# Kernel tuning notes

Hardware: AMD Instinct MI355X
Metric: run time of the kernel (lower is better)

Reference implementation:

```python
import jax, jax.numpy as jnp
import numpy as np

N, E, D, L = 100000, 640000, 128, 5
BN_EPS = 1e-5


def setup_inputs() -> dict:
    key = jax.random.key(0)
    ks = jax.random.split(key, 10)
    x = jax.random.normal(ks[0], (N, D), jnp.float32)
    edge_index = jax.random.randint(ks[1], (2, E), 0, N, dtype=jnp.int32)
    W1 = jax.random.normal(ks[2], (L, D, 2 * D), jnp.float32) / np.float32(np.sqrt(D))
    b1 = jnp.zeros((L, 2 * D), jnp.float32)
    bn1_g = jnp.ones((L, 2 * D), jnp.float32)
    bn1_b = jnp.zeros((L, 2 * D), jnp.float32)
    bn1_m = 0.1 * jax.random.normal(ks[3], (L, 2 * D), jnp.float32)
    bn1_v = jax.random.uniform(ks[4], (L, 2 * D), jnp.float32) + 0.5
    W2 = jax.random.normal(ks[5], (L, 2 * D, D), jnp.float32) / np.float32(np.sqrt(2 * D))
    b2 = jnp.zeros((L, D), jnp.float32)
    bno_g = jnp.ones((L, D), jnp.float32)
    bno_b = jnp.zeros((L, D), jnp.float32)
    bno_m = 0.1 * jax.random.normal(ks[6], (L, D), jnp.float32)
    bno_v = jax.random.uniform(ks[7], (L, D), jnp.float32) + 0.5
    return {"x": x, "edge_index": edge_index, "W1": W1, "b1": b1,
            "bn1_g": bn1_g, "bn1_b": bn1_b, "bn1_m": bn1_m, "bn1_v": bn1_v,
            "W2": W2, "b2": b2,
            "bno_g": bno_g, "bno_b": bno_b, "bno_m": bno_m, "bno_v": bno_v}


def _bn(z, g, b, m, v):
    # BatchNorm1d in eval mode: running stats
    return (z - m) * jax.lax.rsqrt(v + BN_EPS) * g + b


def reference(x, edge_index, W1, b1, bn1_g, bn1_b, bn1_m, bn1_v,
              W2, b2, bno_g, bno_b, bno_m, bno_v):
    src, dst = edge_index[0], edge_index[1]
    h = x
    for l in range(L):
        # GINConv with eps=0: (1+eps)*h_i + sum_{j->i} h_j
        agg = h + jax.ops.segment_sum(h[src], dst, num_segments=N)  # [N, d]
        z = jax.nn.relu(_bn(agg @ W1[l] + b1[l], bn1_g[l], bn1_b[l], bn1_m[l], bn1_v[l]))
        h = _bn(z @ W2[l] + b2[l], bno_g[l], bno_b[l], bno_m[l], bno_v[l])
        if l != L - 1:
            h = jax.nn.relu(h)
        # dropout is identity in eval mode
    return h
```

## Files before the change

kernel.cpp:

```cpp
#include <hip/hip_runtime.h>

#define ND 100000
#define DD 128
#define HH 256
#define EE 640000
#define LL 5

#define GS 152
#define ZS 280
#define OS 136
#define OF 132

typedef __attribute__((ext_vector_type(8))) short short8;
typedef __attribute__((ext_vector_type(4))) short short4v;
typedef __attribute__((ext_vector_type(4))) float f32x4;

static __device__ __forceinline__ short f2bf(float f) {
    unsigned u = __builtin_bit_cast(unsigned, f);
    unsigned r = (u + 0x7fffu + ((u >> 16) & 1u)) >> 16;
    return (short)r;
}
static __device__ __forceinline__ float bf2f(short s) {
    unsigned u = ((unsigned)(unsigned short)s) << 16;
    return __builtin_bit_cast(float, u);
}

__global__ __launch_bounds__(256) void setup(
    const float* __restrict__ W1, const float* __restrict__ b1,
    const float* __restrict__ g1, const float* __restrict__ bb1,
    const float* __restrict__ m1, const float* __restrict__ v1,
    const float* __restrict__ W2, const float* __restrict__ b2,
    const float* __restrict__ g2, const float* __restrict__ bb2,
    const float* __restrict__ m2, const float* __restrict__ v2,
    const float* __restrict__ x, const int* __restrict__ dst,
    short* __restrict__ W1p, float* __restrict__ b1e,
    short* __restrict__ W2p, float* __restrict__ b2e,
    short* __restrict__ hb, int* __restrict__ cnt)
{
    int bx = blockIdx.x;
    int tid = threadIdx.x;
    if (bx < 640) {
        int id = bx * 256 + tid;
        if (id < LL * HH * DD) {
            int l = id >> 15;
            int rem = id & 32767;
            {
                int n = rem >> 7, k = rem & 127;
                float s = g1[l * HH + n] * rsqrtf(v1[l * HH + n] + 1e-5f);
                W1p[id] = f2bf(W1[l * 32768 + k * HH + n] * s);
            }
            {
                int n2 = rem >> 8, k2 = rem & 255;
                float s = g2[l * DD + n2] * rsqrtf(v2[l * DD + n2] + 1e-5f);
                W2p[id] = f2bf(W2[l * 32768 + k2 * DD + n2] * s);
            }
        }
        if (id < LL * HH) {
            float s = g1[id] * rsqrtf(v1[id] + 1e-5f);
            b1e[id] = (b1[id] - m1[id]) * s + bb1[id];
        }
        if (id < LL * DD) {
            float s = g2[id] * rsqrtf(v2[id] + 1e-5f);
            b2e[id] = (b2[id] - m2[id]) * s + bb2[id];
        }
    } else if (bx < 13140) {
        int i = (bx - 640) * 256 + tid;
        float4 v = reinterpret_cast<const float4*>(x)[i];
        short4v s;
        s.x = f2bf(v.x); s.y = f2bf(v.y); s.z = f2bf(v.z); s.w = f2bf(v.w);
        reinterpret_cast<short4v*>(hb)[i] = s;
    } else {
        int e = (bx - 13140) * 256 + tid;
        if (e < EE) atomicAdd(&cnt[dst[e]], 1);
    }
}

__global__ __launch_bounds__(256) void scan_block(int* __restrict__ cnt, int* __restrict__ bsum)
{
    __shared__ int buf[256];
    int tid = threadIdx.x;
    int idx = blockIdx.x * 256 + tid;
    int v = (idx < ND) ? cnt[idx] : 0;
    buf[tid] = v;
    __syncthreads();
    int sum = v;
    for (int off = 1; off < 256; off <<= 1) {
        int t = (tid >= off) ? buf[tid - off] : 0;
        __syncthreads();
        sum += t;
        buf[tid] = sum;
        __syncthreads();
    }
    if (idx < ND) cnt[idx] = sum;
    if (tid == 255) bsum[blockIdx.x] = sum;
}

__global__ __launch_bounds__(256) void apply_offs2(const int* __restrict__ cnt,
                                                   const int* __restrict__ bsum,
                                                   int* __restrict__ rowst)
{
    __shared__ int sred[256];
    int tid = threadIdx.x;
    int partial = 0;
    for (int i = tid; i < blockIdx.x; i += 256) partial += bsum[i];
    sred[tid] = partial;
    __syncthreads();
    for (int off = 128; off > 0; off >>= 1) {
        if (tid < off) sred[tid] += sred[tid + off];
        __syncthreads();
    }
    int boff = sred[0];
    int idx = blockIdx.x * 256 + tid;
    if (idx < ND) rowst[idx + 1] = cnt[idx] + boff;
    if (idx == 0) rowst[0] = 0;
}

__global__ __launch_bounds__(256) void fill_csr(const int* __restrict__ src,
                                                const int* __restrict__ dst,
                                                const int* __restrict__ rowstart,
                                                int* __restrict__ cursor,
                                                int* __restrict__ csr)
{
    int e = blockIdx.x * 256 + threadIdx.x;
    if (e < EE) {
        int d = dst[e];
        int p = atomicAdd(&cursor[d], 1);
        csr[rowstart[d] + p] = src[e];
    }
}

__global__ __launch_bounds__(512, 8) void layer_fused(
    const short* __restrict__ hb_in,
    const int* __restrict__ rowst,
    const int* __restrict__ csr,
    const short* __restrict__ W1l,
    const float* __restrict__ b1l,
    const short* __restrict__ W2l,
    const float* __restrict__ b2l,
    short* __restrict__ hb_out, float* __restrict__ f_out, int last)
{
    __shared__ __attribute__((aligned(16))) short sU[32 * ZS];

    const int tid = threadIdx.x;
    const int r0 = blockIdx.x * 32;
    const int w = tid >> 6;
    const int lane = tid & 63;
    const int quad = lane >> 4;
    const int l16 = lane & 15;

    {
        const int row = tid >> 4;
        const int ch = (tid & 15) * 8;
        const int grow = r0 + row;
        const int s = rowst[grow], e = rowst[grow + 1];
        short8 h0 = *reinterpret_cast<const short8*>(&hb_in[(size_t)grow * DD + ch]);
        float acc[8];
        #pragma unroll
        for (int j = 0; j < 8; ++j) acc[j] = bf2f(h0[j]);

        const int deg = e - s;
        const int nfull = deg >> 2;
        const int rem = deg & 3;
        int i = s;
        short8 ca[4];
        if (nfull) {
            #pragma unroll
            for (int k = 0; k < 4; ++k)
                ca[k] = *reinterpret_cast<const short8*>(&hb_in[(size_t)csr[i + k] * DD + ch]);
            i += 4;
            for (int b = 1; b < nfull; ++b) {
                short8 na[4];
                #pragma unroll
                for (int k = 0; k < 4; ++k)
                    na[k] = *reinterpret_cast<const short8*>(&hb_in[(size_t)csr[i + k] * DD + ch]);
                i += 4;
                #pragma unroll
                for (int j = 0; j < 8; ++j)
                    acc[j] += (bf2f(ca[0][j]) + bf2f(ca[1][j])) + (bf2f(ca[2][j]) + bf2f(ca[3][j]));
                #pragma unroll
                for (int k = 0; k < 4; ++k) ca[k] = na[k];
            }
        }
        short8 t0, t1, t2;
        if (rem > 0) t0 = *reinterpret_cast<const short8*>(&hb_in[(size_t)csr[i] * DD + ch]);
        if (rem > 1) t1 = *reinterpret_cast<const short8*>(&hb_in[(size_t)csr[i + 1] * DD + ch]);
        if (rem > 2) t2 = *reinterpret_cast<const short8*>(&hb_in[(size_t)csr[i + 2] * DD + ch]);
        if (nfull) {
            #pragma unroll
            for (int j = 0; j < 8; ++j)
                acc[j] += (bf2f(ca[0][j]) + bf2f(ca[1][j])) + (bf2f(ca[2][j]) + bf2f(ca[3][j]));
        }
        if (rem > 0) {
            #pragma unroll
            for (int j = 0; j < 8; ++j) acc[j] += bf2f(t0[j]);
        }
        if (rem > 1) {
            #pragma unroll
            for (int j = 0; j < 8; ++j) acc[j] += bf2f(t1[j]);
        }
        if (rem > 2) {
            #pragma unroll
            for (int j = 0; j < 8; ++j) acc[j] += bf2f(t2[j]);
        }
        short8 o;
        #pragma unroll
        for (int j = 0; j < 8; ++j) o[j] = f2bf(acc[j]);
        *reinterpret_cast<short8*>(&sU[row * GS + ch]) = o;
    }
    __syncthreads();

    const f32x4 zero4 = {0.f, 0.f, 0.f, 0.f};
    f32x4 acc1[2][2];
    #pragma unroll
    for (int h = 0; h < 2; ++h)
        #pragma unroll
        for (int nt = 0; nt < 2; ++nt) acc1[h][nt] = zero4;

    const int zr0 = w * 32 + l16;
    short8 a_cur0 = *reinterpret_cast<const short8*>(&W1l[zr0 * DD + quad * 8]);
    short8 a_cur1 = *reinterpret_cast<const short8*>(&W1l[(zr0 + 16) * DD + quad * 8]);

    __builtin_amdgcn_s_setprio(1);
    #pragma unroll
    for (int ks = 0; ks < 4; ++ks) {
        short8 a_n0, a_n1;
        if (ks < 3) {
            a_n0 = *reinterpret_cast<const short8*>(&W1l[zr0 * DD + (ks + 1) * 32 + quad * 8]);
            a_n1 = *reinterpret_cast<const short8*>(&W1l[(zr0 + 16) * DD + (ks + 1) * 32 + quad * 8]);
        }
        int kofs = ks * 32 + quad * 8;
        short8 b0 = *reinterpret_cast<const short8*>(&sU[l16 * GS + kofs]);
        short8 b1 = *reinterpret_cast<const short8*>(&sU[(16 + l16) * GS + kofs]);
        acc1[0][0] = __builtin_amdgcn_mfma_f32_16x16x32_bf16(a_cur0, b0, acc1[0][0], 0, 0, 0);
        acc1[0][1] = __builtin_amdgcn_mfma_f32_16x16x32_bf16(a_cur0, b1, acc1[0][1], 0, 0, 0);
        acc1[1][0] = __builtin_amdgcn_mfma_f32_16x16x32_bf16(a_cur1, b0, acc1[1][0], 0, 0, 0);
        acc1[1][1] = __builtin_amdgcn_mfma_f32_16x16x32_bf16(a_cur1, b1, acc1[1][1], 0, 0, 0);
        a_cur0 = a_n0; a_cur1 = a_n1;
    }
    __builtin_amdgcn_s_setprio(0);

    float4 bi0 = *reinterpret_cast<const float4*>(&b1l[w * 32 + quad * 4]);
    float4 bi1 = *reinterpret_cast<const float4*>(&b1l[w * 32 + 16 + quad * 4]);
    __syncthreads();

    #pragma unroll
    for (int h = 0; h < 2; ++h) {
        float4 bi = h ? bi1 : bi0;
        int zc = w * 32 + h * 16 + quad * 4;
        #pragma unroll
        for (int nt = 0; nt < 2; ++nt) {
            int node = nt * 16 + l16;
            short4v o;
            o.x = f2bf(fmaxf(acc1[h][nt][0] + bi.x, 0.f));
            o.y = f2bf(fmaxf(acc1[h][nt][1] + bi.y, 0.f));
            o.z = f2bf(fmaxf(acc1[h][nt][2] + bi.z, 0.f));
            o.w = f2bf(fmaxf(acc1[h][nt][3] + bi.w, 0.f));
            *reinterpret_cast<short4v*>(&sU[node * ZS + zc]) = o;
        }
    }

    const int orow = w * 16 + l16;
    short8 w_cur = *reinterpret_cast<const short8*>(&W2l[orow * HH + quad * 8]);
    float4 bi2 = *reinterpret_cast<const float4*>(&b2l[w * 16 + quad * 4]);
    __syncthreads();

    f32x4 acc2[2];
    acc2[0] = zero4; acc2[1] = zero4;

    __builtin_amdgcn_s_setprio(1);
    #pragma unroll
    for (int ks = 0; ks < 8; ++ks) {
        short8 w_next;
        if (ks < 7)
            w_next = *reinterpret_cast<const short8*>(&W2l[orow * HH + (ks + 1) * 32 + quad * 8]);
        int kofs = ks * 32 + quad * 8;
        short8 b0 = *reinterpret_cast<const short8*>(&sU[l16 * ZS + kofs]);
        short8 b1 = *reinterpret_cast<const short8*>(&sU[(16 + l16) * ZS + kofs]);
        acc2[0] = __builtin_amdgcn_mfma_f32_16x16x32_bf16(w_cur, b0, acc2[0], 0, 0, 0);
        acc2[1] = __builtin_amdgcn_mfma_f32_16x16x32_bf16(w_cur, b1, acc2[1], 0, 0, 0);
        w_cur = w_next;
    }
    __builtin_amdgcn_s_setprio(0);
    __syncthreads();

    const int oc = w * 16 + quad * 4;
    if (!last) {
        #pragma unroll
        for (int nt = 0; nt < 2; ++nt) {
            int node = nt * 16 + l16;
            short4v o;
            o.x = f2bf(fmaxf(acc2[nt][0] + bi2.x, 0.f));
            o.y = f2bf(fmaxf(acc2[nt][1] + bi2.y, 0.f));
            o.z = f2bf(fmaxf(acc2[nt][2] + bi2.z, 0.f));
            o.w = f2bf(fmaxf(acc2[nt][3] + bi2.w, 0.f));
            *reinterpret_cast<short4v*>(&sU[node * OS + oc]) = o;
        }
        __syncthreads();
        int row = tid >> 4;
        int c8 = (tid & 15) * 8;
        short8 v = *reinterpret_cast<const short8*>(&sU[row * OS + c8]);
        *reinterpret_cast<short8*>(&hb_out[(size_t)(r0 + row) * DD + c8]) = v;
    } else {
        float* fU = reinterpret_cast<float*>(sU);
        #pragma unroll
        for (int nt = 0; nt < 2; ++nt) {
            int node = nt * 16 + l16;
            float4 o;
            o.x = acc2[nt][0] + bi2.x;
            o.y = acc2[nt][1] + bi2.y;
            o.z = acc2[nt][2] + bi2.z;
            o.w = acc2[nt][3] + bi2.w;
            *reinterpret_cast<float4*>(&fU[node * OF + oc]) = o;
        }
        __syncthreads();
        int row = tid >> 4;
        int cb = (tid & 15) * 8;
        float4 v0 = *reinterpret_cast<const float4*>(&fU[row * OF + cb]);
        float4 v1 = *reinterpret_cast<const float4*>(&fU[row * OF + cb + 4]);
        *reinterpret_cast<float4*>(&f_out[(size_t)(r0 + row) * DD + cb]) = v0;
        *reinterpret_cast<float4*>(&f_out[(size_t)(r0 + row) * DD + cb + 4]) = v1;
    }
}

extern "C" void kernel_launch(void* const* d_in, const int* in_sizes, int n_in,
                              void* d_out, int out_size, void* d_ws, size_t ws_size,
                              hipStream_t stream)
{
    const float* x  = (const float*)d_in[0];
    const int* ei   = (const int*)d_in[1];
    const int* src  = ei;
    const int* dst  = ei + EE;
    const float* W1 = (const float*)d_in[2];
    const float* b1 = (const float*)d_in[3];
    const float* g1 = (const float*)d_in[4];
    const float* bb1= (const float*)d_in[5];
    const float* m1 = (const float*)d_in[6];
    const float* v1 = (const float*)d_in[7];
    const float* W2 = (const float*)d_in[8];
    const float* b2 = (const float*)d_in[9];
    const float* g2 = (const float*)d_in[10];
    const float* bb2= (const float*)d_in[11];
    const float* m2 = (const float*)d_in[12];
    const float* v2 = (const float*)d_in[13];

    char* w = (char*)d_ws;
    short* hbufA = (short*)w;
    short* hbufB = (short*)(w + 25600000);
    short* W1p   = (short*)(w + 51200000);
    short* W2p   = (short*)(w + 51527680);
    float* b1e   = (float*)(w + 51855360);
    float* b2e   = (float*)(w + 51860480);
    int*   cnt   = (int*)  (w + 51863040);
    int*   cursor= (int*)  (w + 52263040);
    int*   rowst = (int*)  (w + 52663040);
    int*   csr   = (int*)  (w + 53063072);
    int*   bsum  = (int*)  (w + 55623072);
    float* out   = (float*)d_out;

    hipMemsetAsync(cnt, 0, 800000, stream);
    setup<<<15640, 256, 0, stream>>>(W1, b1, g1, bb1, m1, v1,
                                     W2, b2, g2, bb2, m2, v2,
                                     x, dst, W1p, b1e, W2p, b2e, hbufA, cnt);
    scan_block<<<391, 256, 0, stream>>>(cnt, bsum);
    apply_offs2<<<391, 256, 0, stream>>>(cnt, bsum, rowst);
    fill_csr<<<2500, 256, 0, stream>>>(src, dst, rowst, cursor, csr);

    short* hin = hbufA;
    short* hout = hbufB;
    for (int l = 0; l < LL; ++l) {
        layer_fused<<<3125, 512, 0, stream>>>(hin, rowst, csr,
                                              W1p + l * 32768, b1e + l * HH,
                                              W2p + l * 32768, b2e + l * DD,
                                              hout, out, (l == LL - 1) ? 1 : 0);
        short* t = hin; hin = hout; hout = t;
    }
}
```

Baseline: 549.4 us.

## Sort nodes into degree bins so each layer block gathers rows of similar degree

```diff
diff --git a/kernel.cpp b/kernel.cpp
--- a/kernel.cpp
+++ b/kernel.cpp
@@ -75,12 +75,14 @@
     }
 }
 
-__global__ __launch_bounds__(256) void scan_block(int* __restrict__ cnt, int* __restrict__ bsum)
+__global__ __launch_bounds__(256) void scan_block(int* __restrict__ cnt, int* __restrict__ bsum,
+                                                  int* __restrict__ deghist)
 {
     __shared__ int buf[256];
     int tid = threadIdx.x;
     int idx = blockIdx.x * 256 + tid;
     int v = (idx < ND) ? cnt[idx] : 0;
+    if (idx < ND) atomicAdd(&deghist[v < 63 ? v : 63], 1);
     buf[tid] = v;
     __syncthreads();
     int sum = v;
@@ -97,10 +99,19 @@
 
 __global__ __launch_bounds__(256) void apply_offs2(const int* __restrict__ cnt,
                                                    const int* __restrict__ bsum,
-                                                   int* __restrict__ rowst)
-{
+                                                   int* __restrict__ rowst,
+                                                   const int* __restrict__ deghist,
+                                                   int* __restrict__ binstart)
+{
+    int tid = threadIdx.x;
+    if (blockIdx.x == 391) {
+        if (tid == 0) {
+            int run = 0;
+            for (int d = 63; d >= 0; --d) { binstart[d] = run; run += deghist[d]; }
+        }
+        return;
+    }
     __shared__ int sred[256];
-    int tid = threadIdx.x;
     int partial = 0;
     for (int i = tid; i < blockIdx.x; i += 256) partial += bsum[i];
     sred[tid] = partial;
@@ -119,20 +130,35 @@
                                                 const int* __restrict__ dst,
                                                 const int* __restrict__ rowstart,
                                                 int* __restrict__ cursor,
-                                                int* __restrict__ csr)
-{
-    int e = blockIdx.x * 256 + threadIdx.x;
-    if (e < EE) {
-        int d = dst[e];
-        int p = atomicAdd(&cursor[d], 1);
-        csr[rowstart[d] + p] = src[e];
-    }
-}
-
-__global__ __launch_bounds__(512, 8) void layer_fused(
+                                                int* __restrict__ csr,
+                                                const int* __restrict__ binstart,
+                                                int* __restrict__ bincur,
+                                                int* __restrict__ perm)
+{
+    int bx = blockIdx.x;
+    if (bx < 2500) {
+        int e = bx * 256 + threadIdx.x;
+        if (e < EE) {
+            int d = dst[e];
+            int p = atomicAdd(&cursor[d], 1);
+            csr[rowstart[d] + p] = src[e];
+        }
+    } else {
+        int i = (bx - 2500) * 256 + threadIdx.x;
+        if (i < ND) {
+            int deg = rowstart[i + 1] - rowstart[i];
+            if (deg > 63) deg = 63;
+            int pos = atomicAdd(&bincur[deg], 1);
+            perm[binstart[deg] + pos] = i;
+        }
+    }
+}
+
+__global__ __launch_bounds__(512, 6) void layer_fused(
     const short* __restrict__ hb_in,
     const int* __restrict__ rowst,
     const int* __restrict__ csr,
+    const int* __restrict__ perm,
     const short* __restrict__ W1l,
     const float* __restrict__ b1l,
     const short* __restrict__ W2l,
@@ -140,6 +166,7 @@
     short* __restrict__ hb_out, float* __restrict__ f_out, int last)
 {
     __shared__ __attribute__((aligned(16))) short sU[32 * ZS];
+    __shared__ int sPerm[32];
 
     const int tid = threadIdx.x;
     const int r0 = blockIdx.x * 32;
@@ -151,56 +178,30 @@
     {
         const int row = tid >> 4;
         const int ch = (tid & 15) * 8;
-        const int grow = r0 + row;
+        const int grow = perm[r0 + row];
+        if ((tid & 15) == 0) sPerm[row] = grow;
         const int s = rowst[grow], e = rowst[grow + 1];
         short8 h0 = *reinterpret_cast<const short8*>(&hb_in[(size_t)grow * DD + ch]);
         float acc[8];
         #pragma unroll
         for (int j = 0; j < 8; ++j) acc[j] = bf2f(h0[j]);
 
-        const int deg = e - s;
-        const int nfull = deg >> 2;
-        const int rem = deg & 3;
         int i = s;
-        short8 ca[4];
-        if (nfull) {
+        int deg = e - s;
+        while (deg > 0) {
+            int c = deg < 8 ? deg : 8;
+            short8 a[8];
             #pragma unroll
-            for (int k = 0; k < 4; ++k)
-                ca[k] = *reinterpret_cast<const short8*>(&hb_in[(size_t)csr[i + k] * DD + ch]);
-            i += 4;
-            for (int b = 1; b < nfull; ++b) {
-                short8 na[4];
-                #pragma unroll
-                for (int k = 0; k < 4; ++k)
-                    na[k] = *reinterpret_cast<const short8*>(&hb_in[(size_t)csr[i + k] * DD + ch]);
-                i += 4;
-                #pragma unroll
-                for (int j = 0; j < 8; ++j)
-                    acc[j] += (bf2f(ca[0][j]) + bf2f(ca[1][j])) + (bf2f(ca[2][j]) + bf2f(ca[3][j]));
-                #pragma unroll
-                for (int k = 0; k < 4; ++k) ca[k] = na[k];
-            }
-        }
-        short8 t0, t1, t2;
-        if (rem > 0) t0 = *reinterpret_cast<const short8*>(&hb_in[(size_t)csr[i] * DD + ch]);
-        if (rem > 1) t1 = *reinterpret_cast<const short8*>(&hb_in[(size_t)csr[i + 1] * DD + ch]);
-        if (rem > 2) t2 = *reinterpret_cast<const short8*>(&hb_in[(size_t)csr[i + 2] * DD + ch]);
-        if (nfull) {
+            for (int k = 0; k < 8; ++k)
+                if (k < c)
+                    a[k] = *reinterpret_cast<const short8*>(&hb_in[(size_t)csr[i + k] * DD + ch]);
             #pragma unroll
-            for (int j = 0; j < 8; ++j)
-                acc[j] += (bf2f(ca[0][j]) + bf2f(ca[1][j])) + (bf2f(ca[2][j]) + bf2f(ca[3][j]));
-        }
-        if (rem > 0) {
-            #pragma unroll
-            for (int j = 0; j < 8; ++j) acc[j] += bf2f(t0[j]);
-        }
-        if (rem > 1) {
-            #pragma unroll
-            for (int j = 0; j < 8; ++j) acc[j] += bf2f(t1[j]);
-        }
-        if (rem > 2) {
-            #pragma unroll
-            for (int j = 0; j < 8; ++j) acc[j] += bf2f(t2[j]);
+            for (int k = 0; k < 8; ++k)
+                if (k < c) {
+                    #pragma unroll
+                    for (int j = 0; j < 8; ++j) acc[j] += bf2f(a[k][j]);
+                }
+            i += c; deg -= c;
         }
         short8 o;
         #pragma unroll
@@ -299,7 +300,7 @@
         int row = tid >> 4;
         int c8 = (tid & 15) * 8;
         short8 v = *reinterpret_cast<const short8*>(&sU[row * OS + c8]);
-        *reinterpret_cast<short8*>(&hb_out[(size_t)(r0 + row) * DD + c8]) = v;
+        *reinterpret_cast<short8*>(&hb_out[(size_t)sPerm[row] * DD + c8]) = v;
     } else {
         float* fU = reinterpret_cast<float*>(sU);
         #pragma unroll
@@ -317,8 +318,9 @@
         int cb = (tid & 15) * 8;
         float4 v0 = *reinterpret_cast<const float4*>(&fU[row * OF + cb]);
         float4 v1 = *reinterpret_cast<const float4*>(&fU[row * OF + cb + 4]);
-        *reinterpret_cast<float4*>(&f_out[(size_t)(r0 + row) * DD + cb]) = v0;
-        *reinterpret_cast<float4*>(&f_out[(size_t)(r0 + row) * DD + cb + 4]) = v1;
+        float* orow_p = &f_out[(size_t)sPerm[row] * DD + cb];
+        *reinterpret_cast<float4*>(orow_p) = v0;
+        *reinterpret_cast<float4*>(orow_p + 4) = v1;
     }
 }
 
@@ -352,23 +354,27 @@
     float* b2e   = (float*)(w + 51860480);
     int*   cnt   = (int*)  (w + 51863040);
     int*   cursor= (int*)  (w + 52263040);
-    int*   rowst = (int*)  (w + 52663040);
-    int*   csr   = (int*)  (w + 53063072);
-    int*   bsum  = (int*)  (w + 55623072);
+    int*   deghist=(int*)  (w + 52663040);
+    int*   bincur= (int*)  (w + 52663296);
+    int*   binst = (int*)  (w + 52663552);
+    int*   rowst = (int*)  (w + 52663808);
+    int*   csr   = (int*)  (w + 53063840);
+    int*   bsum  = (int*)  (w + 55623840);
+    int*   perm  = (int*)  (w + 55625504);
     float* out   = (float*)d_out;
 
-    hipMemsetAsync(cnt, 0, 800000, stream);
+    hipMemsetAsync(cnt, 0, 800512, stream);
     setup<<<15640, 256, 0, stream>>>(W1, b1, g1, bb1, m1, v1,
                                      W2, b2, g2, bb2, m2, v2,
                                      x, dst, W1p, b1e, W2p, b2e, hbufA, cnt);
-    scan_block<<<391, 256, 0, stream>>>(cnt, bsum);
-    apply_offs2<<<391, 256, 0, stream>>>(cnt, bsum, rowst);
-    fill_csr<<<2500, 256, 0, stream>>>(src, dst, rowst, cursor, csr);
+    scan_block<<<391, 256, 0, stream>>>(cnt, bsum, deghist);
+    apply_offs2<<<392, 256, 0, stream>>>(cnt, bsum, rowst, deghist, binst);
+    fill_csr<<<2891, 256, 0, stream>>>(src, dst, rowst, cursor, csr, binst, bincur, perm);
 
     short* hin = hbufA;
     short* hout = hbufB;
     for (int l = 0; l < LL; ++l) {
-        layer_fused<<<3125, 512, 0, stream>>>(hin, rowst, csr,
+        layer_fused<<<3125, 512, 0, stream>>>(hin, rowst, csr, perm,
                                               W1p + l * 32768, b1e + l * HH,
                                               W2p + l * 32768, b2e + l * DD,
                                               hout, out, (l == LL - 1) ? 1 : 0);
```

Result: slower. 1.272 ms (+131.5%).

## Process two 32-row tiles per block with interleaved gather

Applied to the files above, without the earlier changes.

```diff
diff --git a/kernel.cpp b/kernel.cpp
--- a/kernel.cpp
+++ b/kernel.cpp
@@ -9,7 +9,6 @@
 #define GS 152
 #define ZS 280
 #define OS 136
-#define OF 132
 
 typedef __attribute__((ext_vector_type(8))) short short8;
 typedef __attribute__((ext_vector_type(4))) short short4v;
@@ -129,7 +128,127 @@
     }
 }
 
-__global__ __launch_bounds__(512, 8) void layer_fused(
+static __device__ __forceinline__ void tile_mlp(
+    const short* __restrict__ sG, short* __restrict__ sZ, short* __restrict__ sO,
+    int r0t, int tid,
+    const short* __restrict__ W1l, const float* __restrict__ b1l,
+    const short* __restrict__ W2l, const float* __restrict__ b2l,
+    short* __restrict__ hb_out, float* __restrict__ f_out, int last)
+{
+    const int w = tid >> 6;
+    const int lane = tid & 63;
+    const int quad = lane >> 4;
+    const int l16 = lane & 15;
+    const f32x4 zero4 = {0.f, 0.f, 0.f, 0.f};
+
+    f32x4 acc1[2][2];
+    #pragma unroll
+    for (int h = 0; h < 2; ++h)
+        #pragma unroll
+        for (int nt = 0; nt < 2; ++nt) acc1[h][nt] = zero4;
+
+    const int zr0 = w * 32 + l16;
+    short8 a_cur0 = *reinterpret_cast<const short8*>(&W1l[zr0 * DD + quad * 8]);
+    short8 a_cur1 = *reinterpret_cast<const short8*>(&W1l[(zr0 + 16) * DD + quad * 8]);
+
+    __builtin_amdgcn_s_setprio(1);
+    #pragma unroll
+    for (int ks = 0; ks < 4; ++ks) {
+        short8 a_n0, a_n1;
+        if (ks < 3) {
+            a_n0 = *reinterpret_cast<const short8*>(&W1l[zr0 * DD + (ks + 1) * 32 + quad * 8]);
+            a_n1 = *reinterpret_cast<const short8*>(&W1l[(zr0 + 16) * DD + (ks + 1) * 32 + quad * 8]);
+        }
+        int kofs = ks * 32 + quad * 8;
+        short8 b0 = *reinterpret_cast<const short8*>(&sG[l16 * GS + kofs]);
+        short8 b1 = *reinterpret_cast<const short8*>(&sG[(16 + l16) * GS + kofs]);
+        acc1[0][0] = __builtin_amdgcn_mfma_f32_16x16x32_bf16(a_cur0, b0, acc1[0][0], 0, 0, 0);
+        acc1[0][1] = __builtin_amdgcn_mfma_f32_16x16x32_bf16(a_cur0, b1, acc1[0][1], 0, 0, 0);
+        acc1[1][0] = __builtin_amdgcn_mfma_f32_16x16x32_bf16(a_cur1, b0, acc1[1][0], 0, 0, 0);
+        acc1[1][1] = __builtin_amdgcn_mfma_f32_16x16x32_bf16(a_cur1, b1, acc1[1][1], 0, 0, 0);
+        a_cur0 = a_n0; a_cur1 = a_n1;
+    }
+    __builtin_amdgcn_s_setprio(0);
+
+    float4 bi0 = *reinterpret_cast<const float4*>(&b1l[w * 32 + quad * 4]);
+    float4 bi1 = *reinterpret_cast<const float4*>(&b1l[w * 32 + 16 + quad * 4]);
+    __syncthreads();
+
+    #pragma unroll
+    for (int h = 0; h < 2; ++h) {
+        float4 bi = h ? bi1 : bi0;
+        int zc = w * 32 + h * 16 + quad * 4;
+        #pragma unroll
+        for (int nt = 0; nt < 2; ++nt) {
+            int node = nt * 16 + l16;
+            short4v o;
+            o.x = f2bf(fmaxf(acc1[h][nt][0] + bi.x, 0.f));
+            o.y = f2bf(fmaxf(acc1[h][nt][1] + bi.y, 0.f));
+            o.z = f2bf(fmaxf(acc1[h][nt][2] + bi.z, 0.f));
+            o.w = f2bf(fmaxf(acc1[h][nt][3] + bi.w, 0.f));
+            *reinterpret_cast<short4v*>(&sZ[node * ZS + zc]) = o;
+        }
+    }
+
+    const int orow = w * 16 + l16;
+    short8 w_cur = *reinterpret_cast<const short8*>(&W2l[orow * HH + quad * 8]);
+    float4 bi2 = *reinterpret_cast<const float4*>(&b2l[w * 16 + quad * 4]);
+    __syncthreads();
+
+    f32x4 acc2[2];
+    acc2[0] = zero4; acc2[1] = zero4;
+
+    __builtin_amdgcn_s_setprio(1);
+    #pragma unroll
+    for (int ks = 0; ks < 8; ++ks) {
+        short8 w_next;
+        if (ks < 7)
+            w_next = *reinterpret_cast<const short8*>(&W2l[orow * HH + (ks + 1) * 32 + quad * 8]);
+        int kofs = ks * 32 + quad * 8;
+        short8 b0 = *reinterpret_cast<const short8*>(&sZ[l16 * ZS + kofs]);
+        short8 b1 = *reinterpret_cast<const short8*>(&sZ[(16 + l16) * ZS + kofs]);
+        acc2[0] = __builtin_amdgcn_mfma_f32_16x16x32_bf16(w_cur, b0, acc2[0], 0, 0, 0);
+        acc2[1] = __builtin_amdgcn_mfma_f32_16x16x32_bf16(w_cur, b1, acc2[1], 0, 0, 0);
+        w_cur = w_next;
+    }
+    __builtin_amdgcn_s_setprio(0);
+
+    const int oc = w * 16 + quad * 4;
+    if (!last) {
+        #pragma unroll
+        for (int nt = 0; nt < 2; ++nt) {
+            int node = nt * 16 + l16;
+            short4v o;
+            o.x = f2bf(fmaxf(acc2[nt][0] + bi2.x, 0.f));
+            o.y = f2bf(fmaxf(acc2[nt][1] + bi2.y, 0.f));
+            o.z = f2bf(fmaxf(acc2[nt][2] + bi2.z, 0.f));
+            o.w = f2bf(fmaxf(acc2[nt][3] + bi2.w, 0.f));
+            *reinterpret_cast<short4v*>(&sO[node * OS + oc]) = o;
+        }
+        __syncthreads();
+        int row = tid >> 4;
+        int c8 = (tid & 15) * 8;
+        if (r0t + row < ND) {
+            short8 v = *reinterpret_cast<const short8*>(&sO[row * OS + c8]);
+            *reinterpret_cast<short8*>(&hb_out[(size_t)(r0t + row) * DD + c8]) = v;
+        }
+    } else {
+        #pragma unroll
+        for (int nt = 0; nt < 2; ++nt) {
+            int node = r0t + nt * 16 + l16;
+            if (node < ND) {
+                float4 o;
+                o.x = acc2[nt][0] + bi2.x;
+                o.y = acc2[nt][1] + bi2.y;
+                o.z = acc2[nt][2] + bi2.z;
+                o.w = acc2[nt][3] + bi2.w;
+                *reinterpret_cast<float4*>(&f_out[(size_t)node * DD + oc]) = o;
+            }
+        }
+    }
+}
+
+__global__ __launch_bounds__(512, 4) void layer_fused(
     const short* __restrict__ hb_in,
     const int* __restrict__ rowst,
     const int* __restrict__ csr,
@@ -139,187 +258,74 @@
     const float* __restrict__ b2l,
     short* __restrict__ hb_out, float* __restrict__ f_out, int last)
 {
-    __shared__ __attribute__((aligned(16))) short sU[32 * ZS];
+    __shared__ __attribute__((aligned(16))) short sGA[32 * GS];
+    __shared__ __attribute__((aligned(16))) short sGB[32 * GS];
+    __shared__ __attribute__((aligned(16))) short sZ[32 * ZS];
 
     const int tid = threadIdx.x;
-    const int r0 = blockIdx.x * 32;
-    const int w = tid >> 6;
-    const int lane = tid & 63;
-    const int quad = lane >> 4;
-    const int l16 = lane & 15;
+    const int r0 = blockIdx.x * 64;
 
     {
         const int row = tid >> 4;
         const int ch = (tid & 15) * 8;
-        const int grow = r0 + row;
-        const int s = rowst[grow], e = rowst[grow + 1];
-        short8 h0 = *reinterpret_cast<const short8*>(&hb_in[(size_t)grow * DD + ch]);
-        float acc[8];
-        #pragma unroll
-        for (int j = 0; j < 8; ++j) acc[j] = bf2f(h0[j]);
-
-        const int deg = e - s;
-        const int nfull = deg >> 2;
-        const int rem = deg & 3;
-        int i = s;
-        short8 ca[4];
-        if (nfull) {
+        const int rA = r0 + row;
+        const int rB = r0 + 32 + row;
+
+        int sA = 0, dA = 0, sB = 0, dB = 0;
+        if (rA < ND) { sA = rowst[rA]; dA = rowst[rA + 1] - sA; }
+        if (rB < ND) { sB = rowst[rB]; dB = rowst[rB + 1] - sB; }
+
+        float accA[8], accB[8];
+        {
+            short8 hA, hB;
+            if (rA < ND) hA = *reinterpret_cast<const short8*>(&hb_in[(size_t)rA * DD + ch]);
+            if (rB < ND) hB = *reinterpret_cast<const short8*>(&hb_in[(size_t)rB * DD + ch]);
+            #pragma unroll
+            for (int j = 0; j < 8; ++j) accA[j] = (rA < ND) ? bf2f(hA[j]) : 0.f;
+            #pragma unroll
+            for (int j = 0; j < 8; ++j) accB[j] = (rB < ND) ? bf2f(hB[j]) : 0.f;
+        }
+
+        int iA = sA, iB = sB;
+        while (dA > 0 || dB > 0) {
+            int cA = dA < 4 ? dA : 4;
+            int cB = dB < 4 ? dB : 4;
+            short8 a[4], b[4];
             #pragma unroll
             for (int k = 0; k < 4; ++k)
-                ca[k] = *reinterpret_cast<const short8*>(&hb_in[(size_t)csr[i + k] * DD + ch]);
-            i += 4;
-            for (int b = 1; b < nfull; ++b) {
-                short8 na[4];
-                #pragma unroll
-                for (int k = 0; k < 4; ++k)
-                    na[k] = *reinterpret_cast<const short8*>(&hb_in[(size_t)csr[i + k] * DD + ch]);
-                i += 4;
-                #pragma unroll
-                for (int j = 0; j < 8; ++j)
-                    acc[j] += (bf2f(ca[0][j]) + bf2f(ca[1][j])) + (bf2f(ca[2][j]) + bf2f(ca[3][j]));
-                #pragma unroll
-                for (int k = 0; k < 4; ++k) ca[k] = na[k];
-            }
-        }
-        short8 t0, t1, t2;
-        if (rem > 0) t0 = *reinterpret_cast<const short8*>(&hb_in[(size_t)csr[i] * DD + ch]);
-        if (rem > 1) t1 = *reinterpret_cast<const short8*>(&hb_in[(size_t)csr[i + 1] * DD + ch]);
-        if (rem > 2) t2 = *reinterpret_cast<const short8*>(&hb_in[(size_t)csr[i + 2] * DD + ch]);
-        if (nfull) {
-            #pragma unroll
-            for (int j = 0; j < 8; ++j)
-                acc[j] += (bf2f(ca[0][j]) + bf2f(ca[1][j])) + (bf2f(ca[2][j]) + bf2f(ca[3][j]));
-        }
-        if (rem > 0) {
-            #pragma unroll
-            for (int j = 0; j < 8; ++j) acc[j] += bf2f(t0[j]);
-        }
-        if (rem > 1) {
-            #pragma unroll
-            for (int j = 0; j < 8; ++j) acc[j] += bf2f(t1[j]);
-        }
-        if (rem > 2) {
-            #pragma unroll
-            for (int j = 0; j < 8; ++j) acc[j] += bf2f(t2[j]);
-        }
-        short8 o;
-        #pragma unroll
-        for (int j = 0; j < 8; ++j) o[j] = f2bf(acc[j]);
-        *reinterpret_cast<short8*>(&sU[row * GS + ch]) = o;
-    }
-    __syncthreads();
-
-    const f32x4 zero4 = {0.f, 0.f, 0.f, 0.f};
-    f32x4 acc1[2][2];
-    #pragma unroll
-    for (int h = 0; h < 2; ++h)
-        #pragma unroll
-        for (int nt = 0; nt < 2; ++nt) acc1[h][nt] = zero4;
-
-    const int zr0 = w * 32 + l16;
-    short8 a_cur0 = *reinterpret_cast<const short8*>(&W1l[zr0 * DD + quad * 8]);
-    short8 a_cur1 = *reinterpret_cast<const short8*>(&W1l[(zr0 + 16) * DD + quad * 8]);
-
-    __builtin_amdgcn_s_setprio(1);
-    #pragma unroll
-    for (int ks = 0; ks < 4; ++ks) {
-        short8 a_n0, a_n1;
-        if (ks < 3) {
-            a_n0 = *reinterpret_cast<const short8*>(&W1l[zr0 * DD + (ks + 1) * 32 + quad * 8]);
-            a_n1 = *reinterpret_cast<const short8*>(&W1l[(zr0 + 16) * DD + (ks + 1) * 32 + quad * 8]);
-        }
-        int kofs = ks * 32 + quad * 8;
-        short8 b0 = *reinterpret_cast<const short8*>(&sU[l16 * GS + kofs]);
-        short8 b1 = *reinterpret_cast<const short8*>(&sU[(16 + l16) * GS + kofs]);
-        acc1[0][0] = __builtin_amdgcn_mfma_f32_16x16x32_bf16(a_cur0, b0, acc1[0][0], 0, 0, 0);
-        acc1[0][1] = __builtin_amdgcn_mfma_f32_16x16x32_bf16(a_cur0, b1, acc1[0][1], 0, 0, 0);
-        acc1[1][0] = __builtin_amdgcn_mfma_f32_16x16x32_bf16(a_cur1, b0, acc1[1][0], 0, 0, 0);
-        acc1[1][1] = __builtin_amdgcn_mfma_f32_16x16x32_bf16(a_cur1, b1, acc1[1][1], 0, 0, 0);
-        a_cur0 = a_n0; a_cur1 = a_n1;
-    }
-    __builtin_amdgcn_s_setprio(0);
-
-    float4 bi0 = *reinterpret_cast<const float4*>(&b1l[w * 32 + quad * 4]);
-    float4 bi1 = *reinterpret_cast<const float4*>(&b1l[w * 32 + 16 + quad * 4]);
-    __syncthreads();
-
-    #pragma unroll
-    for (int h = 0; h < 2; ++h) {
-        float4 bi = h ? bi1 : bi0;
-        int zc = w * 32 + h * 16 + quad * 4;
-        #pragma unroll
-        for (int nt = 0; nt < 2; ++nt) {
-            int node = nt * 16 + l16;
-            short4v o;
-            o.x = f2bf(fmaxf(acc1[h][nt][0] + bi.x, 0.f));
-            o.y = f2bf(fmaxf(acc1[h][nt][1] + bi.y, 0.f));
-            o.z = f2bf(fmaxf(acc1[h][nt][2] + bi.z, 0.f));
-            o.w = f2bf(fmaxf(acc1[h][nt][3] + bi.w, 0.f));
-            *reinterpret_cast<short4v*>(&sU[node * ZS + zc]) = o;
-        }
-    }
-
-    const int orow = w * 16 + l16;
-    short8 w_cur = *reinterpret_cast<const short8*>(&W2l[orow * HH + quad * 8]);
-    float4 bi2 = *reinterpret_cast<const float4*>(&b2l[w * 16 + quad * 4]);
-    __syncthreads();
-
-    f32x4 acc2[2];
-    acc2[0] = zero4; acc2[1] = zero4;
-
-    __builtin_amdgcn_s_setprio(1);
-    #pragma unroll
-    for (int ks = 0; ks < 8; ++ks) {
-        short8 w_next;
-        if (ks < 7)
-            w_next = *reinterpret_cast<const short8*>(&W2l[orow * HH + (ks + 1) * 32 + quad * 8]);
-        int kofs = ks * 32 + quad * 8;
-        short8 b0 = *reinterpret_cast<const short8*>(&sU[l16 * ZS + kofs]);
-        short8 b1 = *reinterpret_cast<const short8*>(&sU[(16 + l16) * ZS + kofs]);
-        acc2[0] = __builtin_amdgcn_mfma_f32_16x16x32_bf16(w_cur, b0, acc2[0], 0, 0, 0);
-        acc2[1] = __builtin_amdgcn_mfma_f32_16x16x32_bf16(w_cur, b1, acc2[1], 0, 0, 0);
-        w_cur = w_next;
-    }
-    __builtin_amdgcn_s_setprio(0);
-    __syncthreads();
-
-    const int oc = w * 16 + quad * 4;
-    if (!last) {
-        #pragma unroll
-        for (int nt = 0; nt < 2; ++nt) {
-            int node = nt * 16 + l16;
-            short4v o;
-            o.x = f2bf(fmaxf(acc2[nt][0] + bi2.x, 0.f));
-            o.y = f2bf(fmaxf(acc2[nt][1] + bi2.y, 0.f));
-            o.z = f2bf(fmaxf(acc2[nt][2] + bi2.z, 0.f));
-            o.w = f2bf(fmaxf(acc2[nt][3] + bi2.w, 0.f));
-            *reinterpret_cast<short4v*>(&sU[node * OS + oc]) = o;
-        }
-        __syncthreads();
-        int row = tid >> 4;
-        int c8 = (tid & 15) * 8;
-        short8 v = *reinterpret_cast<const short8*>(&sU[row * OS + c8]);
-        *reinterpret_cast<short8*>(&hb_out[(size_t)(r0 + row) * DD + c8]) = v;
-    } else {
-        float* fU = reinterpret_cast<float*>(sU);
-        #pragma unroll
-        for (int nt = 0; nt < 2; ++nt) {
-            int node = nt * 16 + l16;
-            float4 o;
-            o.x = acc2[nt][0] + bi2.x;
-            o.y = acc2[nt][1] + bi2.y;
-            o.z = acc2[nt][2] + bi2.z;
-            o.w = acc2[nt][3] + bi2.w;
-            *reinterpret_cast<float4*>(&fU[node * OF + oc]) = o;
-        }
-        __syncthreads();
-        int row = tid >> 4;
-        int cb = (tid & 15) * 8;
-        float4 v0 = *reinterpret_cast<const float4*>(&fU[row * OF + cb]);
-        float4 v1 = *reinterpret_cast<const float4*>(&fU[row * OF + cb + 4]);
-        *reinterpret_cast<float4*>(&f_out[(size_t)(r0 + row) * DD + cb]) = v0;
-        *reinterpret_cast<float4*>(&f_out[(size_t)(r0 + row) * DD + cb + 4]) = v1;
-    }
+                if (k < cA)
+                    a[k] = *reinterpret_cast<const short8*>(&hb_in[(size_t)csr[iA + k] * DD + ch]);
+            #pragma unroll
+            for (int k = 0; k < 4; ++k)
+                if (k < cB)
+                    b[k] = *reinterpret_cast<const short8*>(&hb_in[(size_t)csr[iB + k] * DD + ch]);
+            #pragma unroll
+            for (int k = 0; k < 4; ++k)
+                if (k < cA) {
+                    #pragma unroll
+                    for (int j = 0; j < 8; ++j) accA[j] += bf2f(a[k][j]);
+                }
+            #pragma unroll
+            for (int k = 0; k < 4; ++k)
+                if (k < cB) {
+                    #pragma unroll
+                    for (int j = 0; j < 8; ++j) accB[j] += bf2f(b[k][j]);
+                }
+            iA += cA; dA -= cA;
+            iB += cB; dB -= cB;
+        }
+        short8 oA, oB;
+        #pragma unroll
+        for (int j = 0; j < 8; ++j) oA[j] = f2bf(accA[j]);
+        #pragma unroll
+        for (int j = 0; j < 8; ++j) oB[j] = f2bf(accB[j]);
+        *reinterpret_cast<short8*>(&sGA[row * GS + ch]) = oA;
+        *reinterpret_cast<short8*>(&sGB[row * GS + ch]) = oB;
+    }
+    __syncthreads();
+
+    tile_mlp(sGA, sZ, sGA, r0,      tid, W1l, b1l, W2l, b2l, hb_out, f_out, last);
+    tile_mlp(sGB, sZ, sGB, r0 + 32, tid, W1l, b1l, W2l, b2l, hb_out, f_out, last);
 }
 
 extern "C" void kernel_launch(void* const* d_in, const int* in_sizes, int n_in,
@@ -368,7 +374,7 @@
     short* hin = hbufA;
     short* hout = hbufB;
     for (int l = 0; l < LL; ++l) {
-        layer_fused<<<3125, 512, 0, stream>>>(hin, rowst, csr,
+        layer_fused<<<1563, 512, 0, stream>>>(hin, rowst, csr,
                                               W1p + l * 32768, b1e + l * HH,
                                               W2p + l * 32768, b2e + l * DD,
                                               hout, out, (l == LL - 1) ? 1 : 0);
```

New measurement: 672.0 us. +22.3%, slower.
